# Kernel optimization log

Measured on AMD Instinct MI355X. Metric: run time of the kernel, lower is better.

The kernel has to match this reference:

```python
import jax, jax.numpy as jnp
import numpy as np

B, L, C, H, DK = 2, 2048, 256, 8, 32  # batch, seq, feaSize, multiNum, dk


def setup_inputs() -> dict:
    key = jax.random.key(0)
    ks = jax.random.split(key, 11)
    w = lambda k, shape: jax.random.normal(k, shape, dtype=jnp.float32) * 0.02
    return {
        'qx': jax.random.normal(ks[0], (B, L, C), dtype=jnp.float32),
        'kx': jax.random.normal(ks[1], (B, L, C), dtype=jnp.float32),
        'vx': jax.random.normal(ks[2], (B, L, C), dtype=jnp.float32),
        'WQ': w(ks[3], (C, H * DK)), 'bQ': w(ks[4], (H * DK,)),
        'WK': w(ks[5], (C, H * DK)), 'bK': w(ks[6], (H * DK,)),
        'WV': w(ks[7], (C, H * DK)), 'bV': w(ks[8], (H * DK,)),
        'WO': w(ks[9], (H * DK, C)), 'bO': w(ks[10], (C,)),
    }


def reference(qx, kx, vx, WQ, bQ, WK, bK, WV, bV, WO, bO):
    b, l, c = qx.shape
    # projections -> (B, H, L, DK)
    q = (qx @ WQ + bQ).reshape(b, l, H, DK).transpose(0, 2, 1, 3)
    k = (kx @ WK + bK).reshape(b, l, H, DK).transpose(0, 2, 1, 3)
    v = (vx @ WV + bV).reshape(b, l, H, DK).transpose(0, 2, 1, 3)

    g = jnp.array([0, l - 1])  # global rows / cols
    scores = jnp.zeros((b, H, l, l), dtype=q.dtype)
    # global rows: q[0], q[L-1] attend to everything
    scores = scores.at[:, :, g, :].set(jnp.einsum('bhgd,bhld->bhgl', q[:, :, g, :], k))
    # global cols: everything attends to k[0], k[L-1]
    scores = scores.at[:, :, :, g].set(jnp.einsum('bhld,bhgd->bhlg', q, k[:, :, g, :]))
    # sliding window: super-diag, sub-diag, main diag (dot products along DK)
    i = jnp.arange(l - 1)
    scores = scores.at[:, :, i, i + 1].set(jnp.sum(q[:, :, :-1] * k[:, :, 1:], axis=-1))
    scores = scores.at[:, :, i + 1, i].set(jnp.sum(q[:, :, 1:] * k[:, :, :-1], axis=-1))
    d = jnp.arange(l)
    scores = scores.at[:, :, d, d].set(jnp.sum(q * k, axis=-1))
    # NOTE: the torch random-block write `scores[:,:,r,:][:,:,:,r] = ...` writes
    # into a copy (chained advanced indexing) and is therefore a no-op; we
    # faithfully omit it. Unfilled positions keep score 0 (not -inf), as in torch.
    scores = scores / np.float32(np.sqrt(DK))
    alpha = jax.nn.softmax(scores, axis=3)
    z = jnp.einsum('bhlm,bhmd->bhld', alpha, v)
    z = z.transpose(0, 2, 1, 3).reshape(b, l, H * DK)
    return z @ WO + bO
```

## Files before the change

### kernel.cpp

```cpp
#include <hip/hip_runtime.h>
#include <hip/hip_bf16.h>

#define B_   2
#define L_   2048
#define C_   256
#define H_   8
#define DK_  32
#define HD_  256
#define RSQRT_DK 0.17677669529663687f

typedef __attribute__((ext_vector_type(8))) short bf16x8;
typedef __attribute__((ext_vector_type(4))) float f32x4;
typedef __attribute__((ext_vector_type(4))) unsigned int u32x4;

__device__ __forceinline__ unsigned short f2bf(float x) {
    unsigned int u = __float_as_uint(x);
    u += 0x7fffu + ((u >> 16) & 1u);
    return (unsigned short)(u >> 16);
}
__device__ __forceinline__ float bf2f(unsigned short h) {
    return __uint_as_float((unsigned int)h << 16);
}

__device__ __forceinline__ uint2 split2(float x0, float x1) {
    __hip_bfloat162 h2 = __float22bfloat162_rn(make_float2(x0, x1));
    unsigned hu; __builtin_memcpy(&hu, &h2, 4);
    const float e0 = __uint_as_float(hu << 16);
    const float e1 = __uint_as_float(hu & 0xffff0000u);
    __hip_bfloat162 l2 = __float22bfloat162_rn(make_float2(x0 - e0, x1 - e1));
    unsigned lu; __builtin_memcpy(&lu, &l2, 4);
    return make_uint2(hu, lu);
}
__device__ __forceinline__ bf16x8 as_bf16x8(u32x4 v) {
    bf16x8 r; __builtin_memcpy(&r, &v, 16); return r;
}

#define WT_IDX(n, k) (((n) << 8) + (((((k) >> 3) ^ ((n) & 7))) << 3) + ((k) & 7))

__device__ __forceinline__ void stage_wT_512(
    const float* __restrict__ W, int n0, int tid,
    short* __restrict__ WTh, short* __restrict__ WTl)
{
    const int n  = tid & 63;
    const int kc = tid >> 6;
    #pragma unroll
    for (int c8 = 0; c8 < 4; ++c8) {
        const int k0 = kc * 32 + c8 * 8;
        u32x4 hv, lv;
        #pragma unroll
        for (int e = 0; e < 4; ++e) {
            const float x0 = W[(size_t)(k0 + 2 * e)     * HD_ + n0 + n];
            const float x1 = W[(size_t)(k0 + 2 * e + 1) * HD_ + n0 + n];
            const uint2 hl = split2(x0, x1);
            hv[e] = hl.x; lv[e] = hl.y;
        }
        const int o = (n << 8) + ((((k0 >> 3) ^ (n & 7))) << 3);
        *reinterpret_cast<u32x4*>(&WTh[o]) = hv;
        *reinterpret_cast<u32x4*>(&WTl[o]) = lv;
    }
}

__device__ __forceinline__ void stage_wT_copy(
    const unsigned short* __restrict__ wTp, int n0, int tid,
    short* __restrict__ WTh, short* __restrict__ WTl)
{
    #pragma unroll
    for (int it = 0; it < 8; ++it) {
        const int c = tid + it * 256;
        const int n = c >> 5, k8 = c & 31;
        const size_t go = (size_t)(n0 + n) * 256 + k8 * 8;
        const int o = (n << 8) + ((k8 ^ (n & 7)) << 3);
        *reinterpret_cast<bf16x8*>(&WTh[o]) = *reinterpret_cast<const bf16x8*>(&wTp[go]);
        *reinterpret_cast<bf16x8*>(&WTl[o]) = *reinterpret_cast<const bf16x8*>(&wTp[65536 + go]);
    }
}

__global__ __launch_bounds__(512) void gemm_qkv_fused(
    const float* __restrict__ qx, const float* __restrict__ kx, const float* __restrict__ vx,
    const float* __restrict__ WQ, const float* __restrict__ bQ,
    const float* __restrict__ WK, const float* __restrict__ bK,
    const float* __restrict__ WV, const float* __restrict__ bV,
    const float* __restrict__ WO, unsigned short* __restrict__ wT,
    float* __restrict__ q, float* __restrict__ k, float* __restrict__ v,
    float* __restrict__ part)
{
    const int bx = blockIdx.x;
    const int yy = blockIdx.y;
    const int tid = threadIdx.x;

    if (yy == 12) {
        if (tid < 256) {
            const int n  = bx * 8 + (tid >> 5);
            const int k8 = (tid & 31) * 8;
            u32x4 hv, lv;
            #pragma unroll
            for (int e = 0; e < 4; ++e) {
                const float x0 = WO[(size_t)(k8 + 2 * e)     * HD_ + n];
                const float x1 = WO[(size_t)(k8 + 2 * e + 1) * HD_ + n];
                const uint2 hl = split2(x0, x1);
                hv[e] = hl.x; lv[e] = hl.y;
            }
            *reinterpret_cast<u32x4*>(&wT[(size_t)n * 256 + k8])         = hv;
            *reinterpret_cast<u32x4*>(&wT[65536 + (size_t)n * 256 + k8]) = lv;
        }
        return;
    }

    const int proj = yy >> 2, nt = yy & 3;
    const float* A    = proj == 0 ? qx : (proj == 1 ? kx : vx);
    const float* W    = proj == 0 ? WQ : (proj == 1 ? WK : WV);
    const float* bias = proj == 0 ? bQ : (proj == 1 ? bK : bV);
    float* out        = proj == 0 ? q  : (proj == 1 ? k  : v);
    const int n0 = nt * 64;

    __shared__ short WTh[64 * 256];
    __shared__ short WTl[64 * 256];
    __shared__ float red[8][4][16];

    stage_wT_512(W, n0, tid, WTh, WTl);
    __syncthreads();

    const int w  = tid >> 6;
    const int l  = tid & 63;
    const int lm = l & 15, lk8 = (l >> 4) * 8, cr = (l >> 4) * 4;
    const int R  = bx * 128 + w * 16;

    f32x4 acc[4];
    #pragma unroll
    for (int nf = 0; nf < 4; ++nf) acc[nf] = (f32x4){0.f, 0.f, 0.f, 0.f};

    float4 Ab[2][2];
    #define LOAD_A(buf, ks)                                                          \
    {                                                                                \
        const float* p0 = &A[(size_t)(R + lm) * C_ + (ks) * 32 + lk8];               \
        Ab[buf][0] = *reinterpret_cast<const float4*>(p0);                           \
        Ab[buf][1] = *reinterpret_cast<const float4*>(p0 + 4);                       \
    }
    LOAD_A(0, 0)
    LOAD_A(1, 1)

    #pragma unroll
    for (int ks = 0; ks < 8; ++ks) {
        const int cur = ks & 1;
        bf16x8 ah, al;
        {
            float4 v0 = Ab[cur][0], v1 = Ab[cur][1];
            u32x4 hq, lq;
            const uint2 r0 = split2(v0.x, v0.y);
            const uint2 r1 = split2(v0.z, v0.w);
            const uint2 r2 = split2(v1.x, v1.y);
            const uint2 r3 = split2(v1.z, v1.w);
            hq[0] = r0.x; lq[0] = r0.y;
            hq[1] = r1.x; lq[1] = r1.y;
            hq[2] = r2.x; lq[2] = r2.y;
            hq[3] = r3.x; lq[3] = r3.y;
            ah = as_bf16x8(hq);
            al = as_bf16x8(lq);
        }
        if (ks < 6) LOAD_A(cur, ks + 2)
        #pragma unroll
        for (int nf = 0; nf < 4; ++nf) {
            const int o = WT_IDX(nf * 16 + lm, ks * 32 + lk8);
            const bf16x8 b_h = *reinterpret_cast<const bf16x8*>(&WTh[o]);
            const bf16x8 b_l = *reinterpret_cast<const bf16x8*>(&WTl[o]);
            acc[nf] = __builtin_amdgcn_mfma_f32_16x16x32_bf16(ah, b_h, acc[nf], 0, 0, 0);
            acc[nf] = __builtin_amdgcn_mfma_f32_16x16x32_bf16(ah, b_l, acc[nf], 0, 0, 0);
            acc[nf] = __builtin_amdgcn_mfma_f32_16x16x32_bf16(al, b_h, acc[nf], 0, 0, 0);
        }
    }
    #undef LOAD_A

    #pragma unroll
    for (int nf = 0; nf < 4; ++nf) {
        const int col = n0 + nf * 16 + lm;
        const int h = col >> 5, d = col & 31;
        const float bb = bias[col];
        #pragma unroll
        for (int r = 0; r < 4; ++r) {
            const int m = R + cr + r;
            const int b = m >> 11, lrow = m & (L_ - 1);
            out[((size_t)(b * H_ + h) * L_ + lrow) * DK_ + d] = acc[nf][r] + bb;
        }
    }

    if (proj == 2) {
        float sl[4];
        #pragma unroll
        for (int nf = 0; nf < 4; ++nf) {
            float s = acc[nf][0] + acc[nf][1] + acc[nf][2] + acc[nf][3];
            s += __shfl_xor(s, 16);
            s += __shfl_xor(s, 32);
            sl[nf] = s;
        }
        if (l < 16) {
            #pragma unroll
            for (int nf = 0; nf < 4; ++nf) red[w][nf][l] = sl[nf];
        }
        __syncthreads();
        if (tid < 64) {
            const int nf = tid >> 4, lmm = tid & 15;
            float tot = 0.f;
            #pragma unroll
            for (int ww = 0; ww < 8; ++ww) tot += red[ww][nf][lmm];
            const int col = n0 + nf * 16 + lmm;
            tot += 128.f * bias[col];
            const int h = col >> 5, d = col & 31;
            const int bh = (bx >> 4) * H_ + h;
            part[((size_t)bh * 32 + d) * 16 + (bx & 15)] = tot;
        }
    }
}

__global__ __launch_bounds__(128) void attn_main(
    const float* __restrict__ q, const float* __restrict__ k,
    const float* __restrict__ v, const float* __restrict__ part,
    float* __restrict__ pm, float* __restrict__ pZ, float* __restrict__ pzv,
    unsigned short* __restrict__ zh, unsigned short* __restrict__ zl)
{
    __shared__ float Sf[324];

    const int blk = blockIdx.x;
    const int t = threadIdx.x;

    if (blk < 256) {
        const int bh = blk >> 4, c = blk & 15;
        const int base = c * 128;
        const float* qb = q + (size_t)bh * L_ * DK_;
        const float* kb = k + (size_t)bh * L_ * DK_;
        const float* vb = v + (size_t)bh * L_ * DK_;
        float* vs_sh = Sf;

        if (t < 32) {
            const float4* pp = reinterpret_cast<const float4*>(&part[((size_t)bh * 32 + t) * 16]);
            float4 pa = pp[0], pb = pp[1], pc = pp[2], pd = pp[3];
            vs_sh[t] = pa.x + pa.y + pa.z + pa.w + pb.x + pb.y + pb.z + pb.w
                     + pc.x + pc.y + pc.z + pc.w + pd.x + pd.y + pd.z + pd.w;
        }
        __syncthreads();

        const int i = base + 1 + t;
        if (i <= L_ - 2) {
            float qr[32];
            {
                const float4* qp = reinterpret_cast<const float4*>(&qb[(size_t)i * DK_]);
                #pragma unroll
                for (int u2 = 0; u2 < 8; ++u2) {
                    float4 x = qp[u2];
                    qr[u2 * 4 + 0] = x.x; qr[u2 * 4 + 1] = x.y;
                    qr[u2 * 4 + 2] = x.z; qr[u2 * 4 + 3] = x.w;
                }
            }
            const int rows[5] = {0, i - 1, i, i + 1, L_ - 1};
            float sv[5];
            #pragma unroll
            for (int jj = 0; jj < 5; ++jj) {
                const float4* kp = reinterpret_cast<const float4*>(&kb[(size_t)rows[jj] * DK_]);
                float p = 0.f;
                #pragma unroll
                for (int u2 = 0; u2 < 8; ++u2) {
                    float4 kv = kp[u2];
                    p += qr[u2 * 4 + 0] * kv.x + qr[u2 * 4 + 1] * kv.y
                       + qr[u2 * 4 + 2] * kv.z + qr[u2 * 4 + 3] * kv.w;
                }
                sv[jj] = p * RSQRT_DK;
            }
            const bool v1 = (i != 1), v3 = (i != L_ - 2);
            float m = fmaxf(0.f, sv[0]);
            m = fmaxf(m, sv[2]); m = fmaxf(m, sv[4]);
            if (v1) m = fmaxf(m, sv[1]);
            if (v3) m = fmaxf(m, sv[3]);
            float e[5];
            e[0] = __expf(sv[0] - m);
            e[1] = v1 ? __expf(sv[1] - m) : 0.f;
            e[2] = __expf(sv[2] - m);
            e[3] = v3 ? __expf(sv[3] - m) : 0.f;
            e[4] = __expf(sv[4] - m);
            const int ns = 3 + (int)v1 + (int)v3;
            const float e0 = __expf(-m);
            const float Z = e[0] + e[1] + e[2] + e[3] + e[4] + (float)(L_ - ns) * e0;
            const float rZ = 1.f / Z;
            const float f1 = v1 ? 1.f : 0.f, f3 = v3 ? 1.f : 0.f;

            const float4* vp0 = reinterpret_cast<const float4*>(&vb[0]);
            const float4* vp1 = reinterpret_cast<const float4*>(&vb[(size_t)rows[1] * DK_]);
            const float4* vp2 = reinterpret_cast<const float4*>(&vb[(size_t)i * DK_]);
            const float4* vp3 = reinterpret_cast<const float4*>(&vb[(size_t)rows[3] * DK_]);
            const float4* vp4 = reinterpret_cast<const float4*>(&vb[(size_t)(L_ - 1) * DK_]);

            u32x4 zhq[4], zlq[4];
            #pragma unroll
            for (int u2 = 0; u2 < 8; ++u2) {
                float4 x0 = vp0[u2], x1 = vp1[u2], x2 = vp2[u2], x3 = vp3[u2], x4 = vp4[u2];
                float a0[4] = {x0.x, x0.y, x0.z, x0.w};
                float a1[4] = {x1.x, x1.y, x1.z, x1.w};
                float a2[4] = {x2.x, x2.y, x2.z, x2.w};
                float a3[4] = {x3.x, x3.y, x3.z, x3.w};
                float a4[4] = {x4.x, x4.y, x4.z, x4.w};
                float zd4[4];
                #pragma unroll
                for (int e2 = 0; e2 < 4; ++e2) {
                    const int d = u2 * 4 + e2;
                    const float num = e[0] * a0[e2] + e[1] * a1[e2] + e[2] * a2[e2]
                                    + e[3] * a3[e2] + e[4] * a4[e2];
                    const float vp_ = a0[e2] + f1 * a1[e2] + a2[e2] + f3 * a3[e2] + a4[e2];
                    zd4[e2] = (num + e0 * (vs_sh[d] - vp_)) * rZ;
                }
                const uint2 p0 = split2(zd4[0], zd4[1]);
                const uint2 p1 = split2(zd4[2], zd4[3]);
                zhq[u2 >> 1][(u2 & 1) * 2 + 0] = p0.x;
                zhq[u2 >> 1][(u2 & 1) * 2 + 1] = p1.x;
                zlq[u2 >> 1][(u2 & 1) * 2 + 0] = p0.y;
                zlq[u2 >> 1][(u2 & 1) * 2 + 1] = p1.y;
            }
            const int b = bh >> 3, h = bh & 7;
            const size_t o = (size_t)(b * L_ + i) * HD_ + h * DK_;
            #pragma unroll
            for (int u4 = 0; u4 < 4; ++u4) {
                *reinterpret_cast<u32x4*>(&zh[o + u4 * 8]) = zhq[u4];
                *reinterpret_cast<u32x4*>(&zl[o + u4 * 8]) = zlq[u4];
            }
        }
    } else {
        const int blk2 = blk - 256;
        const int bh = blk2 >> 5;
        const int pair = (blk2 >> 4) & 1;
        const int chunk = blk2 & 15;
        const int r = pair ? (L_ - 1) : 0;
        const int j0 = chunk * 128;
        const float* qb = q + (size_t)bh * L_ * DK_;
        const float* kb = k + (size_t)bh * L_ * DK_;
        const float* vb = v + (size_t)bh * L_ * DK_;

        float* qs  = Sf;
        float* sc  = Sf + 32;
        float* red = Sf + 160;
        float* pzs = Sf + 192;

        if (t < 32) qs[t] = qb[(size_t)r * DK_ + t];
        __syncthreads();

        const int j = j0 + t;
        const float4* kr = reinterpret_cast<const float4*>(&kb[(size_t)j * DK_]);
        float p = 0.f;
        #pragma unroll
        for (int u = 0; u < 8; ++u) {
            float4 kv = kr[u];
            p += qs[u * 4 + 0] * kv.x + qs[u * 4 + 1] * kv.y
               + qs[u * 4 + 2] * kv.z + qs[u * 4 + 3] * kv.w;
        }
        p *= RSQRT_DK;

        float lm = p;
        #pragma unroll
        for (int off = 32; off; off >>= 1) lm = fmaxf(lm, __shfl_xor(lm, off, 64));
        if ((t & 63) == 0) red[t >> 6] = lm;
        __syncthreads();
        const float m = fmaxf(red[0], red[1]);

        const float e = __expf(p - m);
        sc[t] = e;
        float ls = e;
        #pragma unroll
        for (int off = 32; off; off >>= 1) ls += __shfl_xor(ls, off, 64);
        if ((t & 63) == 0) red[2 + (t >> 6)] = ls;
        __syncthreads();
        const float Zc = red[2] + red[3];

        const int d = t & 31, g = t >> 5;
        float acc = 0.f;
        #pragma unroll 4
        for (int jj = 0; jj < 32; ++jj)
            acc += sc[g * 32 + jj] * vb[(size_t)(j0 + g * 32 + jj) * DK_ + d];
        pzs[g * 32 + d] = acc;
        __syncthreads();
        if (g == 0) {
            const float s2 = pzs[d] + pzs[32 + d] + pzs[64 + d] + pzs[96 + d];
            pzv[(size_t)blk2 * 32 + d] = s2;
        }
        if (t == 0) { pm[blk2] = m; pZ[blk2] = Zc; }
    }
}

__global__ __launch_bounds__(256) void gemm_out_fused(
    const unsigned short* __restrict__ zh_c, unsigned short* __restrict__ zh,
    unsigned short* __restrict__ zl,
    const float* __restrict__ pm, const float* __restrict__ pZ,
    const float* __restrict__ pzv,
    const unsigned short* __restrict__ wT, const float* __restrict__ bO,
    float* __restrict__ out)
{
    const int bx = blockIdx.x;
    const int nt = blockIdx.y;
    const int n0 = nt * 64;

    __shared__ short WTh[64 * 256];
    __shared__ short WTl[64 * 256];

    const int tid = threadIdx.x;
    stage_wT_copy(wT, n0, tid, WTh, WTl);

    int zrow = -1;
    if      (bx == 0)  zrow = 0;
    else if (bx == 31) zrow = L_ - 1;
    else if (bx == 32) zrow = L_;
    else if (bx == 63) zrow = 2 * L_ - 1;
    if (zrow >= 0) {
        const int h = tid >> 5, d = tid & 31;
        const int b = zrow >> 11;
        const int r = zrow & (L_ - 1);
        const int pair = r ? 1 : 0;
        const int rowIdx = (b * H_ + h) * 2 + pair;
        const int base = rowIdx * 16;
        float m = -1e30f;
        #pragma unroll
        for (int c = 0; c < 16; ++c) m = fmaxf(m, pm[base + c]);
        float Z = 0.f, zd = 0.f;
        #pragma unroll
        for (int c = 0; c < 16; ++c) {
            const float w2 = __expf(pm[base + c] - m);
            Z  += pZ[base + c] * w2;
            zd += pzv[(size_t)(base + c) * 32 + d] * w2;
        }
        zd /= Z;
        const size_t o = (size_t)zrow * HD_ + h * DK_ + d;
        const unsigned short hb = f2bf(zd);
        zh[o] = hb;
        zl[o] = f2bf(zd - bf2f(hb));
    }
    __syncthreads();

    const int w  = tid >> 6;
    const int l  = tid & 63;
    const int lm = l & 15, lk8 = (l >> 4) * 8, cr = (l >> 4) * 4;
    const int R  = bx * 64 + w * 16;

    f32x4 acc[4];
    #pragma unroll
    for (int nf = 0; nf < 4; ++nf) acc[nf] = (f32x4){0.f, 0.f, 0.f, 0.f};

    bf16x8 Ah[2], Al[2];
    #define LOAD_Z(buf, ks)                                                          \
    {                                                                                \
        const size_t o = (size_t)(R + lm) * HD_ + (ks) * 32 + lk8;                   \
        Ah[buf] = *reinterpret_cast<const bf16x8*>(&zh_c[o]);                        \
        Al[buf] = *reinterpret_cast<const bf16x8*>(&zl[o]);                          \
    }
    LOAD_Z(0, 0)
    LOAD_Z(1, 1)

    #pragma unroll
    for (int ks = 0; ks < 8; ++ks) {
        const int cur = ks & 1;
        const bf16x8 a_h = Ah[cur], a_l = Al[cur];
        if (ks < 6) LOAD_Z(cur, ks + 2)
        #pragma unroll
        for (int nf = 0; nf < 4; ++nf) {
            const int o = WT_IDX(nf * 16 + lm, ks * 32 + lk8);
            const bf16x8 b_h = *reinterpret_cast<const bf16x8*>(&WTh[o]);
            const bf16x8 b_l = *reinterpret_cast<const bf16x8*>(&WTl[o]);
            acc[nf] = __builtin_amdgcn_mfma_f32_16x16x32_bf16(a_h, b_h, acc[nf], 0, 0, 0);
            acc[nf] = __builtin_amdgcn_mfma_f32_16x16x32_bf16(a_h, b_l, acc[nf], 0, 0, 0);
            acc[nf] = __builtin_amdgcn_mfma_f32_16x16x32_bf16(a_l, b_h, acc[nf], 0, 0, 0);
        }
    }
    #undef LOAD_Z

    #pragma unroll
    for (int nf = 0; nf < 4; ++nf) {
        const int col = n0 + nf * 16 + lm;
        const float bb = bO[col];
        #pragma unroll
        for (int r = 0; r < 4; ++r) {
            const int m = R + cr + r;
            out[(size_t)m * HD_ + col] = acc[nf][r] + bb;
        }
    }
}

extern "C" void kernel_launch(void* const* d_in, const int* in_sizes, int n_in,
                              void* d_out, int out_size, void* d_ws, size_t ws_size,
                              hipStream_t stream)
{
    const float* qx = (const float*)d_in[0];
    const float* kx = (const float*)d_in[1];
    const float* vx = (const float*)d_in[2];
    const float* WQ = (const float*)d_in[3];
    const float* bQ = (const float*)d_in[4];
    const float* WK = (const float*)d_in[5];
    const float* bK = (const float*)d_in[6];
    const float* WV = (const float*)d_in[7];
    const float* bV = (const float*)d_in[8];
    const float* WO = (const float*)d_in[9];
    const float* bO = (const float*)d_in[10];
    float* out = (float*)d_out;

    char* wsb = (char*)d_ws;
    float*          q    = (float*)(wsb);
    float*          k    = (float*)(wsb + (4u  << 20));
    float*          v    = (float*)(wsb + (8u  << 20));
    unsigned short* zh   = (unsigned short*)(wsb + (12u << 20));
    unsigned short* zl   = (unsigned short*)(wsb + (14u << 20));
    float*          part = (float*)(wsb + (16u << 20));
    float*          pm   = (float*)(wsb + (16u << 20) + (1u << 16));
    float*          pZ   = pm + 512;
    float*          pzv  = pm + 1024;
    unsigned short* wT   = (unsigned short*)(wsb + (17u << 20));

    gemm_qkv_fused<<<dim3(32, 13), 512, 0, stream>>>(qx, kx, vx, WQ, bQ, WK, bK, WV, bV, WO, wT, q, k, v, part);
    attn_main<<<768, 128, 0, stream>>>(q, k, v, part, pm, pZ, pzv, zh, zl);
    gemm_out_fused<<<dim3(64, 4), 256, 0, stream>>>(zh, zh, zl, pm, pZ, pzv, wT, bO, out);
}
```

Baseline: 32.80 us.

## Split attention rows across four lanes and widen global-row chunks

Result: slower. 33.61 us (+2.5%).

```diff
diff --git a/kernel.cpp b/kernel.cpp
--- a/kernel.cpp
+++ b/kernel.cpp
@@ -211,20 +211,20 @@
     }
 }
 
-__global__ __launch_bounds__(128) void attn_main(
+__global__ __launch_bounds__(256) void attn_main(
     const float* __restrict__ q, const float* __restrict__ k,
     const float* __restrict__ v, const float* __restrict__ part,
     float* __restrict__ pm, float* __restrict__ pZ, float* __restrict__ pzv,
     unsigned short* __restrict__ zh, unsigned short* __restrict__ zl)
 {
-    __shared__ float Sf[324];
+    __shared__ float Sf[560];
 
     const int blk = blockIdx.x;
     const int t = threadIdx.x;
 
-    if (blk < 256) {
-        const int bh = blk >> 4, c = blk & 15;
-        const int base = c * 128;
+    if (blk < 512) {
+        const int bh = blk >> 5, c = blk & 31;
+        const int base = c * 64;
         const float* qb = q + (size_t)bh * L_ * DK_;
         const float* kb = k + (size_t)bh * L_ * DK_;
         const float* vb = v + (size_t)bh * L_ * DK_;
@@ -238,30 +238,26 @@
         }
         __syncthreads();
 
-        const int i = base + 1 + t;
+        const int rq = t >> 2, sub = t & 3, d0 = sub * 8;
+        const int i = base + 1 + rq;
         if (i <= L_ - 2) {
-            float qr[32];
+            float qr[8];
             {
-                const float4* qp = reinterpret_cast<const float4*>(&qb[(size_t)i * DK_]);
-                #pragma unroll
-                for (int u2 = 0; u2 < 8; ++u2) {
-                    float4 x = qp[u2];
-                    qr[u2 * 4 + 0] = x.x; qr[u2 * 4 + 1] = x.y;
-                    qr[u2 * 4 + 2] = x.z; qr[u2 * 4 + 3] = x.w;
-                }
+                const float4* qp = reinterpret_cast<const float4*>(&qb[(size_t)i * DK_ + d0]);
+                float4 x0 = qp[0], x1 = qp[1];
+                qr[0] = x0.x; qr[1] = x0.y; qr[2] = x0.z; qr[3] = x0.w;
+                qr[4] = x1.x; qr[5] = x1.y; qr[6] = x1.z; qr[7] = x1.w;
             }
             const int rows[5] = {0, i - 1, i, i + 1, L_ - 1};
             float sv[5];
             #pragma unroll
             for (int jj = 0; jj < 5; ++jj) {
-                const float4* kp = reinterpret_cast<const float4*>(&kb[(size_t)rows[jj] * DK_]);
-                float p = 0.f;
-                #pragma unroll
-                for (int u2 = 0; u2 < 8; ++u2) {
-                    float4 kv = kp[u2];
-                    p += qr[u2 * 4 + 0] * kv.x + qr[u2 * 4 + 1] * kv.y
-                       + qr[u2 * 4 + 2] * kv.z + qr[u2 * 4 + 3] * kv.w;
-                }
+                const float4* kp = reinterpret_cast<const float4*>(&kb[(size_t)rows[jj] * DK_ + d0]);
+                float4 k0 = kp[0], k1 = kp[1];
+                float p = qr[0] * k0.x + qr[1] * k0.y + qr[2] * k0.z + qr[3] * k0.w
+                        + qr[4] * k1.x + qr[5] * k1.y + qr[6] * k1.z + qr[7] * k1.w;
+                p += __shfl_xor(p, 1);
+                p += __shfl_xor(p, 2);
                 sv[jj] = p * RSQRT_DK;
             }
             const bool v1 = (i != 1), v3 = (i != L_ - 2);
@@ -281,60 +277,64 @@
             const float rZ = 1.f / Z;
             const float f1 = v1 ? 1.f : 0.f, f3 = v3 ? 1.f : 0.f;
 
-            const float4* vp0 = reinterpret_cast<const float4*>(&vb[0]);
-            const float4* vp1 = reinterpret_cast<const float4*>(&vb[(size_t)rows[1] * DK_]);
-            const float4* vp2 = reinterpret_cast<const float4*>(&vb[(size_t)i * DK_]);
-            const float4* vp3 = reinterpret_cast<const float4*>(&vb[(size_t)rows[3] * DK_]);
-            const float4* vp4 = reinterpret_cast<const float4*>(&vb[(size_t)(L_ - 1) * DK_]);
-
-            u32x4 zhq[4], zlq[4];
+            const float4* vp0 = reinterpret_cast<const float4*>(&vb[0 + d0]);
+            const float4* vp1 = reinterpret_cast<const float4*>(&vb[(size_t)rows[1] * DK_ + d0]);
+            const float4* vp2 = reinterpret_cast<const float4*>(&vb[(size_t)i * DK_ + d0]);
+            const float4* vp3 = reinterpret_cast<const float4*>(&vb[(size_t)rows[3] * DK_ + d0]);
+            const float4* vp4 = reinterpret_cast<const float4*>(&vb[(size_t)(L_ - 1) * DK_ + d0]);
+            float a0[8], a1[8], a2[8], a3[8], a4[8];
+            {
+                float4 y0 = vp0[0], y1 = vp0[1];
+                a0[0]=y0.x; a0[1]=y0.y; a0[2]=y0.z; a0[3]=y0.w; a0[4]=y1.x; a0[5]=y1.y; a0[6]=y1.z; a0[7]=y1.w;
+                y0 = vp1[0]; y1 = vp1[1];
+                a1[0]=y0.x; a1[1]=y0.y; a1[2]=y0.z; a1[3]=y0.w; a1[4]=y1.x; a1[5]=y1.y; a1[6]=y1.z; a1[7]=y1.w;
+                y0 = vp2[0]; y1 = vp2[1];
+                a2[0]=y0.x; a2[1]=y0.y; a2[2]=y0.z; a2[3]=y0.w; a2[4]=y1.x; a2[5]=y1.y; a2[6]=y1.z; a2[7]=y1.w;
+                y0 = vp3[0]; y1 = vp3[1];
+                a3[0]=y0.x; a3[1]=y0.y; a3[2]=y0.z; a3[3]=y0.w; a3[4]=y1.x; a3[5]=y1.y; a3[6]=y1.z; a3[7]=y1.w;
+                y0 = vp4[0]; y1 = vp4[1];
+                a4[0]=y0.x; a4[1]=y0.y; a4[2]=y0.z; a4[3]=y0.w; a4[4]=y1.x; a4[5]=y1.y; a4[6]=y1.z; a4[7]=y1.w;
+            }
+            float zd[8];
             #pragma unroll
-            for (int u2 = 0; u2 < 8; ++u2) {
-                float4 x0 = vp0[u2], x1 = vp1[u2], x2 = vp2[u2], x3 = vp3[u2], x4 = vp4[u2];
-                float a0[4] = {x0.x, x0.y, x0.z, x0.w};
-                float a1[4] = {x1.x, x1.y, x1.z, x1.w};
-                float a2[4] = {x2.x, x2.y, x2.z, x2.w};
-                float a3[4] = {x3.x, x3.y, x3.z, x3.w};
-                float a4[4] = {x4.x, x4.y, x4.z, x4.w};
-                float zd4[4];
-                #pragma unroll
-                for (int e2 = 0; e2 < 4; ++e2) {
-                    const int d = u2 * 4 + e2;
-                    const float num = e[0] * a0[e2] + e[1] * a1[e2] + e[2] * a2[e2]
-                                    + e[3] * a3[e2] + e[4] * a4[e2];
-                    const float vp_ = a0[e2] + f1 * a1[e2] + a2[e2] + f3 * a3[e2] + a4[e2];
-                    zd4[e2] = (num + e0 * (vs_sh[d] - vp_)) * rZ;
-                }
-                const uint2 p0 = split2(zd4[0], zd4[1]);
-                const uint2 p1 = split2(zd4[2], zd4[3]);
-                zhq[u2 >> 1][(u2 & 1) * 2 + 0] = p0.x;
-                zhq[u2 >> 1][(u2 & 1) * 2 + 1] = p1.x;
-                zlq[u2 >> 1][(u2 & 1) * 2 + 0] = p0.y;
-                zlq[u2 >> 1][(u2 & 1) * 2 + 1] = p1.y;
+            for (int e2 = 0; e2 < 8; ++e2) {
+                const int d = d0 + e2;
+                const float num = e[0] * a0[e2] + e[1] * a1[e2] + e[2] * a2[e2]
+                                + e[3] * a3[e2] + e[4] * a4[e2];
+                const float vp_ = a0[e2] + f1 * a1[e2] + a2[e2] + f3 * a3[e2] + a4[e2];
+                zd[e2] = (num + e0 * (vs_sh[d] - vp_)) * rZ;
+            }
+            u32x4 hq, lq;
+            {
+                const uint2 p0 = split2(zd[0], zd[1]);
+                const uint2 p1 = split2(zd[2], zd[3]);
+                const uint2 p2 = split2(zd[4], zd[5]);
+                const uint2 p3 = split2(zd[6], zd[7]);
+                hq[0] = p0.x; lq[0] = p0.y;
+                hq[1] = p1.x; lq[1] = p1.y;
+                hq[2] = p2.x; lq[2] = p2.y;
+                hq[3] = p3.x; lq[3] = p3.y;
             }
             const int b = bh >> 3, h = bh & 7;
-            const size_t o = (size_t)(b * L_ + i) * HD_ + h * DK_;
-            #pragma unroll
-            for (int u4 = 0; u4 < 4; ++u4) {
-                *reinterpret_cast<u32x4*>(&zh[o + u4 * 8]) = zhq[u4];
-                *reinterpret_cast<u32x4*>(&zl[o + u4 * 8]) = zlq[u4];
-            }
+            const size_t o = (size_t)(b * L_ + i) * HD_ + h * DK_ + d0;
+            *reinterpret_cast<u32x4*>(&zh[o]) = hq;
+            *reinterpret_cast<u32x4*>(&zl[o]) = lq;
         }
     } else {
-        const int blk2 = blk - 256;
-        const int bh = blk2 >> 5;
-        const int pair = (blk2 >> 4) & 1;
-        const int chunk = blk2 & 15;
+        const int blk2 = blk - 512;
+        const int bh = blk2 >> 4;
+        const int pair = (blk2 >> 3) & 1;
+        const int chunk = blk2 & 7;
         const int r = pair ? (L_ - 1) : 0;
-        const int j0 = chunk * 128;
+        const int j0 = chunk * 256;
         const float* qb = q + (size_t)bh * L_ * DK_;
         const float* kb = k + (size_t)bh * L_ * DK_;
         const float* vb = v + (size_t)bh * L_ * DK_;
 
         float* qs  = Sf;
         float* sc  = Sf + 32;
-        float* red = Sf + 160;
-        float* pzs = Sf + 192;
+        float* red = Sf + 288;
+        float* pzs = Sf + 296;
 
         if (t < 32) qs[t] = qb[(size_t)r * DK_ + t];
         __syncthreads();
@@ -355,16 +355,16 @@
         for (int off = 32; off; off >>= 1) lm = fmaxf(lm, __shfl_xor(lm, off, 64));
         if ((t & 63) == 0) red[t >> 6] = lm;
         __syncthreads();
-        const float m = fmaxf(red[0], red[1]);
+        const float m = fmaxf(fmaxf(red[0], red[1]), fmaxf(red[2], red[3]));
 
         const float e = __expf(p - m);
         sc[t] = e;
         float ls = e;
         #pragma unroll
         for (int off = 32; off; off >>= 1) ls += __shfl_xor(ls, off, 64);
-        if ((t & 63) == 0) red[2 + (t >> 6)] = ls;
+        if ((t & 63) == 0) red[4 + (t >> 6)] = ls;
         __syncthreads();
-        const float Zc = red[2] + red[3];
+        const float Zc = red[4] + red[5] + red[6] + red[7];
 
         const int d = t & 31, g = t >> 5;
         float acc = 0.f;
@@ -374,7 +374,9 @@
         pzs[g * 32 + d] = acc;
         __syncthreads();
         if (g == 0) {
-            const float s2 = pzs[d] + pzs[32 + d] + pzs[64 + d] + pzs[96 + d];
+            float s2 = 0.f;
+            #pragma unroll
+            for (int gg = 0; gg < 8; ++gg) s2 += pzs[gg * 32 + d];
             pzv[(size_t)blk2 * 32 + d] = s2;
         }
         if (t == 0) { pm[blk2] = m; pZ[blk2] = Zc; }
@@ -410,13 +412,13 @@
         const int r = zrow & (L_ - 1);
         const int pair = r ? 1 : 0;
         const int rowIdx = (b * H_ + h) * 2 + pair;
-        const int base = rowIdx * 16;
+        const int base = rowIdx * 8;
         float m = -1e30f;
         #pragma unroll
-        for (int c = 0; c < 16; ++c) m = fmaxf(m, pm[base + c]);
+        for (int c = 0; c < 8; ++c) m = fmaxf(m, pm[base + c]);
         float Z = 0.f, zd = 0.f;
         #pragma unroll
-        for (int c = 0; c < 16; ++c) {
+        for (int c = 0; c < 8; ++c) {
             const float w2 = __expf(pm[base + c] - m);
             Z  += pZ[base + c] * w2;
             zd += pzv[(size_t)(base + c) * 32 + d] * w2;
@@ -507,6 +509,6 @@
     unsigned short* wT   = (unsigned short*)(wsb + (17u << 20));
 
     gemm_qkv_fused<<<dim3(32, 13), 512, 0, stream>>>(qx, kx, vx, WQ, bQ, WK, bK, WV, bV, WO, wT, q, k, v, part);
-    attn_main<<<768, 128, 0, stream>>>(q, k, v, part, pm, pZ, pzv, zh, zl);
+    attn_main<<<768, 256, 0, stream>>>(q, k, v, part, pm, pZ, pzv, zh, zl);
     gemm_out_fused<<<dim3(64, 4), 256, 0, stream>>>(zh, zh, zl, pm, pZ, pzv, wT, bO, out);
 }
```
